# Kernel tuning notes

Measured on AMD Instinct MI355X. Metric: run time of the kernel, lower is better.

## Reference

```python
import jax, jax.numpy as jnp
import numpy as np

FEATURE_DIM = 1024
MAX_DEPTH = 32
HID = 128
N = 32768


def setup_inputs() -> dict:
    key = jax.random.key(0)
    ks = jax.random.split(key, 16)
    d = FEATURE_DIM
    s = 0.02
    return {
        "features": jax.random.normal(ks[0], (N, d), jnp.float32),
        "depths": jax.random.randint(ks[1], (N,), 0, MAX_DEPTH),
        "pos_emb": jax.random.normal(ks[2], (MAX_DEPTH, d), jnp.float32) * s,
        "aW1": jax.random.normal(ks[3], (HID, 2 * d), jnp.float32) * s,
        "ab1": jnp.zeros((HID,), jnp.float32),
        "aW2": jax.random.normal(ks[4], (1, HID), jnp.float32) * s,
        "ab2": jnp.zeros((1,), jnp.float32),
        "uW1": jax.random.normal(ks[5], (d, 2 * d), jnp.float32) * s,
        "ub1": jnp.zeros((d,), jnp.float32),
        "uW2": jax.random.normal(ks[6], (d, d), jnp.float32) * s,
        "ub2": jnp.zeros((d,), jnp.float32),
        "gW": jax.random.normal(ks[7], (d, 2 * d), jnp.float32) * s,
        "gb": jnp.zeros((d,), jnp.float32),
    }


def reference(features, depths, pos_emb, aW1, ab1, aW2, ab2,
              uW1, ub1, uW2, ub2, gW, gb):
    # add position embeddings (depths clamped to [0, MAX_DEPTH-1])
    dep = jnp.clip(depths, 0, MAX_DEPTH - 1)
    f = features + pos_emb[dep]                       # [N, d]
    target = f[0:1]                                    # [1, d]
    path = f[1:]                                       # [N-1, d]

    # attention MLP over all path states at once (vectorizes the torch loop)
    tb = jnp.broadcast_to(target, path.shape)          # [N-1, d]
    comb = jnp.concatenate([tb, path], axis=1)         # [N-1, 2d]
    h = jax.nn.relu(comb @ aW1.T + ab1)                # [N-1, 128]
    attn = jax.nn.sigmoid(h @ aW2.T + ab2)             # [N-1, 1]

    s = attn.sum()
    attn = jnp.where(s > 0, attn / s, attn)

    agg = (path * attn).sum(axis=0, keepdims=True)     # [1, d]
    c2 = jnp.concatenate([target, agg], axis=1)        # [1, 2d]
    gate = jax.nn.sigmoid(c2 @ gW.T + gb)
    upd = jax.nn.relu(c2 @ uW1.T + ub1) @ uW2.T + ub2
    updated_target = target + gate * upd
    return jnp.concatenate([updated_target, path], axis=0)
```

## Files before the change

kernel.cpp:

```cpp
#include <hip/hip_runtime.h>

#define DNUM 1024
#define HIDN 128
#define NTOT 32768
#define MR 32
#define NBLK 1024

#define T_OFF 0
#define P0_OFF 1024
#define S_OFF 1152
#define AGG_OFF 1216
#define GATE_OFF 2240
#define U1_OFF 3264
#define W2_FOFF 4288
#define AGGP_OFF (W2_FOFF + 65536)
#define SP_OFF (AGGP_OFF + NBLK * DNUM)
#define WS_NEED ((size_t)(SP_OFF + NBLK) * 4)

typedef __attribute__((ext_vector_type(8))) short short8;
typedef __attribute__((ext_vector_type(4))) float f32x4;

__device__ __forceinline__ unsigned short f2bf(float x) {
  unsigned int u = __builtin_bit_cast(unsigned int, x);
  u = u + 0x7fffu + ((u >> 16) & 1u);
  return (unsigned short)(u >> 16);
}
__device__ __forceinline__ float bf2f(unsigned int bits16) {
  unsigned int u = bits16 << 16;
  return __builtin_bit_cast(float, u);
}

__global__ __launch_bounds__(256) void ka(const float* __restrict__ features,
                                          const int* __restrict__ depths,
                                          const float* __restrict__ pos_emb,
                                          float* __restrict__ ws) {
  int t = threadIdx.x;
  int dep = depths[0];
  dep = dep < 0 ? 0 : (dep > 31 ? 31 : dep);
  float4 fv = *(const float4*)(features + t * 4);
  float4 pe = *(const float4*)(pos_emb + dep * DNUM + t * 4);
  float4 r;
  r.x = fv.x + pe.x; r.y = fv.y + pe.y; r.z = fv.z + pe.z; r.w = fv.w + pe.w;
  *(float4*)(ws + T_OFF + t * 4) = r;
  float4 z = make_float4(0.f, 0.f, 0.f, 0.f);
  *(float4*)(ws + AGG_OFF + t * 4) = z;
  if (t < 64) ws[S_OFF + t] = 0.f;
}

__global__ __launch_bounds__(256) void kaw(const float* __restrict__ aW1,
                                           const float* __restrict__ ab1,
                                           float* __restrict__ ws,
                                           unsigned short* __restrict__ w2) {
  int t = threadIdx.x, bid = blockIdx.x;
  if (bid == 0) {
    __shared__ float ph[256];
    int j = t >> 1, h = t & 1;
    const float* wrow = aW1 + (size_t)j * (2 * DNUM) + h * 512;
    const float* tr = ws + T_OFF + h * 512;
    float p = 0.f;
    for (int k = 0; k < 512; k += 4) {
      float4 wv = *(const float4*)(wrow + k);
      float4 tv = *(const float4*)(tr + k);
      p += wv.x * tv.x + wv.y * tv.y + wv.z * tv.z + wv.w * tv.w;
    }
    ph[t] = p;
    __syncthreads();
    if (t < HIDN) ws[P0_OFF + t] = ab1[t] + ph[t * 2] + ph[t * 2 + 1];
    return;
  }
  int idx = ((bid - 1) * 256 + t) * 4;
  int j = idx >> 10, k = idx & 1023;
  float4 v = *(const float4*)(aW1 + (size_t)j * 2048 + 1024 + k);
  uint2 pk;
  pk.x = (unsigned int)f2bf(v.x) | ((unsigned int)f2bf(v.y) << 16);
  pk.y = (unsigned int)f2bf(v.z) | ((unsigned int)f2bf(v.w) << 16);
  *(uint2*)(w2 + idx) = pk;
}

__global__ __launch_bounds__(512, 4) void kbig(
    const float* __restrict__ features, const int* __restrict__ depths,
    const float* __restrict__ pos_emb, const float* __restrict__ p0,
    const float* __restrict__ aW2, const float* __restrict__ ab2,
    const unsigned short* __restrict__ w2, float* __restrict__ out,
    float* __restrict__ agg, float* __restrict__ sacc,
    float* __restrict__ aggp, float* __restrict__ sp) {
  __shared__ __align__(16) unsigned char ldsA[MR * 2048];
  __shared__ int depsL[MR];
  __shared__ float part[160];
  __shared__ float comb[1024];
  const int t = threadIdx.x;
  const int bid = blockIdx.x;
  const int lane = t & 63;
  const int w = t >> 6;
  const int llo = lane & 15;
  const int lhi = lane >> 4;
  const int tc = t & 255;
  const int th = t >> 8;
  const int col = tc * 4;

  if (t < MR) {
    int fr = 1 + bid * MR + t;
    int dp = (fr < NTOT) ? depths[fr] : 0;
    dp = dp < 0 ? 0 : (dp > 31 ? 31 : dp);
    depsL[t] = dp;
  }
  __syncthreads();

#pragma unroll
  for (int g = 0; g < 2; ++g) {
    float4 fb[8];
#pragma unroll
    for (int q = 0; q < 8; ++q) {
      int i = (g * 8 + q) * 2 + th;
      int fr = 1 + bid * MR + i;
      fb[q] = (fr < NTOT) ? *(const float4*)(features + (size_t)fr * DNUM + col)
                          : make_float4(0.f, 0.f, 0.f, 0.f);
    }
#pragma unroll
    for (int q = 0; q < 8; ++q) {
      int i = (g * 8 + q) * 2 + th;
      int fr = 1 + bid * MR + i;
      float4 f = make_float4(0.f, 0.f, 0.f, 0.f);
      if (fr < NTOT) {
        float4 pe = *(const float4*)(pos_emb + depsL[i] * DNUM + col);
        f.x = fb[q].x + pe.x; f.y = fb[q].y + pe.y;
        f.z = fb[q].z + pe.z; f.w = fb[q].w + pe.w;
        *(float4*)(out + (size_t)fr * DNUM + col) = f;
      }
      uint2 pk;
      pk.x = (unsigned int)f2bf(f.x) | ((unsigned int)f2bf(f.y) << 16);
      pk.y = (unsigned int)f2bf(f.z) | ((unsigned int)f2bf(f.w) << 16);
      int off = (i * 2048 + tc * 8) ^ ((i & 7) << 4);
      *(uint2*)(ldsA + off) = pk;
    }
  }
  __syncthreads();

  const int wm = w >> 2, wn = w & 3;
  f32x4 acc[2];
  acc[0] = (f32x4){0.f, 0.f, 0.f, 0.f};
  acc[1] = (f32x4){0.f, 0.f, 0.f, 0.f};
  const int arow = wm * 16 + llo;
  const int abase = arow * 2048;
  const int aswz = (arow & 7) << 4;
  const unsigned short* bpA = w2 + (size_t)(wn * 32 + llo) * DNUM + lhi * 8;
  const unsigned short* bpB = bpA + 16 * DNUM;

#pragma unroll 4
  for (int kc = 0; kc < 32; ++kc) {
    int kbase = kc * 32;
    short8 av = *(short8*)(ldsA + ((abase + (kbase + lhi * 8) * 2) ^ aswz));
    short8 bv0 = *(const short8*)(bpA + kbase);
    short8 bv1 = *(const short8*)(bpB + kbase);
    acc[0] = __builtin_amdgcn_mfma_f32_16x16x32_bf16(av, bv0, acc[0], 0, 0, 0);
    acc[1] = __builtin_amdgcn_mfma_f32_16x16x32_bf16(av, bv1, acc[1], 0, 0, 0);
  }

  float p0v[2], wv[2];
#pragma unroll
  for (int n = 0; n < 2; ++n) {
    int j = wn * 32 + n * 16 + llo;
    p0v[n] = p0[j];
    wv[n] = aW2[j];
  }
#pragma unroll
  for (int e = 0; e < 4; ++e) {
    float s = 0.f;
#pragma unroll
    for (int n = 0; n < 2; ++n) {
      float h = acc[n][e] + p0v[n];
      h = fmaxf(h, 0.f);
      s += h * wv[n];
    }
    s += __shfl_xor(s, 1);
    s += __shfl_xor(s, 2);
    s += __shfl_xor(s, 4);
    s += __shfl_xor(s, 8);
    if (llo == 0) part[wn * 32 + wm * 16 + lhi * 4 + e] = s;
  }
  __syncthreads();

  if (t < MR) {
    float pre = part[t] + part[32 + t] + part[64 + t] + part[96 + t] + ab2[0];
    int fr = 1 + bid * MR + t;
    float raw = 0.f;
    if (fr < NTOT) raw = 1.f / (1.f + __expf(-pre));
    part[128 + t] = raw;
  }
  __syncthreads();

  float a0 = 0.f, a1 = 0.f, a2 = 0.f, a3 = 0.f;
  for (int lr = th * 16; lr < th * 16 + 16; ++lr) {
    float r = part[128 + lr];
    int off = (lr * 2048 + tc * 8) ^ ((lr & 7) << 4);
    uint2 pk = *(uint2*)(ldsA + off);
    a0 += r * bf2f(pk.x & 0xffffu);
    a1 += r * bf2f(pk.x >> 16);
    a2 += r * bf2f(pk.y & 0xffffu);
    a3 += r * bf2f(pk.y >> 16);
  }
  if (th == 1) {
    comb[tc * 4 + 0] = a0; comb[tc * 4 + 1] = a1;
    comb[tc * 4 + 2] = a2; comb[tc * 4 + 3] = a3;
  }
  __syncthreads();
  if (th == 0) {
    float c0 = a0 + comb[tc * 4 + 0];
    float c1 = a1 + comb[tc * 4 + 1];
    float c2v = a2 + comb[tc * 4 + 2];
    float c3 = a3 + comb[tc * 4 + 3];
    if (aggp) {
      f32x4 v = {c0, c1, c2v, c3};
      *(f32x4*)(aggp + (size_t)bid * DNUM + col) = v;
    } else {
      atomicAdd(agg + col + 0, c0);
      atomicAdd(agg + col + 1, c1);
      atomicAdd(agg + col + 2, c2v);
      atomicAdd(agg + col + 3, c3);
    }
  }
  if (t == 0) {
    float s = 0.f;
    for (int lr = 0; lr < MR; ++lr) s += part[128 + lr];
    if (sp) sp[bid] = s;
    else atomicAdd(sacc + (bid & 63), s);
  }
}

__global__ __launch_bounds__(256) void kred(const float* __restrict__ aggp,
                                            const float* __restrict__ sp,
                                            float* __restrict__ ws) {
  int t = threadIdx.x, bid = blockIdx.x;
  if (bid < 256) {
    int w = t >> 6, lane = t & 63;
    int colIdx = bid * 4 + w;
    float s = 0.f;
#pragma unroll 4
    for (int k = 0; k < 16; ++k) {
      int r = lane + k * 64;
      s += aggp[(size_t)r * DNUM + colIdx];
    }
    s += __shfl_xor(s, 1);
    s += __shfl_xor(s, 2);
    s += __shfl_xor(s, 4);
    s += __shfl_xor(s, 8);
    s += __shfl_xor(s, 16);
    s += __shfl_xor(s, 32);
    if (lane == 0) ws[AGG_OFF + colIdx] = s;
  } else {
    __shared__ float red[256];
    float s = sp[t] + sp[t + 256] + sp[t + 512] + sp[t + 768];
    red[t] = s;
    __syncthreads();
    if (t < 64) {
      float v = red[t] + red[t + 64] + red[t + 128] + red[t + 192];
      v += __shfl_xor(v, 1);
      v += __shfl_xor(v, 2);
      v += __shfl_xor(v, 4);
      v += __shfl_xor(v, 8);
      v += __shfl_xor(v, 16);
      v += __shfl_xor(v, 32);
      if (t == 0) ws[S_OFF] = v;
    }
  }
}

__global__ __launch_bounds__(256) void kc1(const float* __restrict__ gW,
                                           const float* __restrict__ gb,
                                           const float* __restrict__ uW1,
                                           const float* __restrict__ ub1,
                                           float* __restrict__ ws) {
  __shared__ float c2[2048];
  __shared__ float sinv_sh;
  int t = threadIdx.x, bid = blockIdx.x;
  if (t == 0) {
    float s = 0.f;
    for (int i = 0; i < 64; ++i) s += ws[S_OFF + i];
    sinv_sh = (s > 0.f) ? 1.f / s : 1.f;
  }
  __syncthreads();
  float sinv = sinv_sh;
  for (int i = t; i < 2048; i += 256)
    c2[i] = (i < 1024) ? ws[T_OFF + i] : ws[AGG_OFF + i - 1024] * sinv;
  __syncthreads();
  int w = t >> 6, lane = t & 63;
  int isGate = bid < 256;
  int o = (isGate ? bid : bid - 256) * 4 + w;
  const float* W = isGate ? gW : uW1;
  float p = 0.f;
  for (int i = lane; i < 2048; i += 64) p += W[(size_t)o * 2048 + i] * c2[i];
  p += __shfl_xor(p, 1);
  p += __shfl_xor(p, 2);
  p += __shfl_xor(p, 4);
  p += __shfl_xor(p, 8);
  p += __shfl_xor(p, 16);
  p += __shfl_xor(p, 32);
  if (lane == 0) {
    float v = p + (isGate ? gb[o] : ub1[o]);
    v = isGate ? (1.f / (1.f + expf(-v))) : fmaxf(v, 0.f);
    ws[(isGate ? GATE_OFF : U1_OFF) + o] = v;
  }
}

__global__ __launch_bounds__(256) void kc2(const float* __restrict__ uW2,
                                           const float* __restrict__ ub2,
                                           const float* __restrict__ ws,
                                           float* __restrict__ out) {
  __shared__ float u1[1024];
  int t = threadIdx.x, bid = blockIdx.x;
  for (int i = t; i < 1024; i += 256) u1[i] = ws[U1_OFF + i];
  __syncthreads();
  int w = t >> 6, lane = t & 63;
  int o = bid * 4 + w;
  float p = 0.f;
  for (int i = lane; i < 1024; i += 64) p += uW2[(size_t)o * 1024 + i] * u1[i];
  p += __shfl_xor(p, 1);
  p += __shfl_xor(p, 2);
  p += __shfl_xor(p, 4);
  p += __shfl_xor(p, 8);
  p += __shfl_xor(p, 16);
  p += __shfl_xor(p, 32);
  if (lane == 0) {
    float upd = p + ub2[o];
    out[o] = ws[T_OFF + o] + ws[GATE_OFF + o] * upd;
  }
}

extern "C" void kernel_launch(void* const* d_in, const int* in_sizes, int n_in,
                              void* d_out, int out_size, void* d_ws, size_t ws_size,
                              hipStream_t stream) {
  const float* features = (const float*)d_in[0];
  const int* depths = (const int*)d_in[1];
  const float* pos_emb = (const float*)d_in[2];
  const float* aW1 = (const float*)d_in[3];
  const float* ab1 = (const float*)d_in[4];
  const float* aW2 = (const float*)d_in[5];
  const float* ab2 = (const float*)d_in[6];
  const float* uW1 = (const float*)d_in[7];
  const float* ub1 = (const float*)d_in[8];
  const float* uW2 = (const float*)d_in[9];
  const float* ub2 = (const float*)d_in[10];
  const float* gW = (const float*)d_in[11];
  const float* gb = (const float*)d_in[12];
  float* out = (float*)d_out;
  float* ws = (float*)d_ws;
  unsigned short* w2 = (unsigned short*)(ws + W2_FOFF);
  bool useP = ws_size >= WS_NEED;
  float* aggp = useP ? (ws + AGGP_OFF) : nullptr;
  float* sp = useP ? (ws + SP_OFF) : nullptr;

  hipLaunchKernelGGL(ka, dim3(1), dim3(256), 0, stream, features, depths, pos_emb, ws);
  hipLaunchKernelGGL(kaw, dim3(129), dim3(256), 0, stream, aW1, ab1, ws, w2);
  hipLaunchKernelGGL(kbig, dim3(NBLK), dim3(512), 0, stream, features, depths, pos_emb,
                     ws + P0_OFF, aW2, ab2, w2, out, ws + AGG_OFF, ws + S_OFF, aggp, sp);
  if (useP)
    hipLaunchKernelGGL(kred, dim3(257), dim3(256), 0, stream, aggp, sp, ws);
  hipLaunchKernelGGL(kc1, dim3(512), dim3(256), 0, stream, gW, gb, uW1, ub1, ws);
  hipLaunchKernelGGL(kc2, dim3(256), dim3(256), 0, stream, uW2, ub2, ws, out);
}
```

Baseline: 179.1 us.

## Pipeline feature loads with MFMA via double-buffered LDS tiles per block

The main kernel now processes 64 rows per block in four 16-row tiles with double-buffered LDS. The global load of the next tile's features is issued before the current tile's MFMA/attention work, and its LDS write happens after, so memory latency overlaps compute. Each wave now covers 16 hidden units for 16 rows. The grid is halved to 512 blocks, which also halves the partial-aggregate buffer that the reduction kernel reads. In exchange there are more barriers per block, fewer blocks to fill the GPU, and fewer MFMA per wave per tile.

Result: no change. 182.5 us (+1.9%).

```diff
diff --git a/kernel.cpp b/kernel.cpp
--- a/kernel.cpp
+++ b/kernel.cpp
@@ -3,8 +3,10 @@
 #define DNUM 1024
 #define HIDN 128
 #define NTOT 32768
-#define MR 32
-#define NBLK 1024
+#define MR 16
+#define TB 4
+#define ROWS_PB (MR * TB)
+#define NBLKB 512
 
 #define T_OFF 0
 #define P0_OFF 1024
@@ -14,8 +16,8 @@
 #define U1_OFF 3264
 #define W2_FOFF 4288
 #define AGGP_OFF (W2_FOFF + 65536)
-#define SP_OFF (AGGP_OFF + NBLK * DNUM)
-#define WS_NEED ((size_t)(SP_OFF + NBLK) * 4)
+#define SP_OFF (AGGP_OFF + NBLKB * DNUM)
+#define WS_NEED ((size_t)(SP_OFF + NBLKB) * 4)
 
 typedef __attribute__((ext_vector_type(8))) short short8;
 typedef __attribute__((ext_vector_type(4))) float f32x4;
@@ -77,16 +79,15 @@
   *(uint2*)(w2 + idx) = pk;
 }
 
-__global__ __launch_bounds__(512, 4) void kbig(
+__global__ __launch_bounds__(512, 4) void kpipe(
     const float* __restrict__ features, const int* __restrict__ depths,
     const float* __restrict__ pos_emb, const float* __restrict__ p0,
     const float* __restrict__ aW2, const float* __restrict__ ab2,
     const unsigned short* __restrict__ w2, float* __restrict__ out,
     float* __restrict__ agg, float* __restrict__ sacc,
     float* __restrict__ aggp, float* __restrict__ sp) {
-  __shared__ __align__(16) unsigned char ldsA[MR * 2048];
-  __shared__ int depsL[MR];
-  __shared__ float part[160];
+  __shared__ __align__(16) unsigned char lds[2][MR * 2048];
+  __shared__ float part[144];
   __shared__ float comb[1024];
   const int t = threadIdx.x;
   const int bid = blockIdx.x;
@@ -97,32 +98,28 @@
   const int tc = t & 255;
   const int th = t >> 8;
   const int col = tc * 4;
-
-  if (t < MR) {
-    int fr = 1 + bid * MR + t;
-    int dp = (fr < NTOT) ? depths[fr] : 0;
-    dp = dp < 0 ? 0 : (dp > 31 ? 31 : dp);
-    depsL[t] = dp;
-  }
-  __syncthreads();
-
-#pragma unroll
-  for (int g = 0; g < 2; ++g) {
-    float4 fb[8];
+  const int rowbase = 1 + bid * ROWS_PB;
+
+  float4 fb[8];
+
+  auto FLOAD = [&](int tt) {
 #pragma unroll
     for (int q = 0; q < 8; ++q) {
-      int i = (g * 8 + q) * 2 + th;
-      int fr = 1 + bid * MR + i;
+      int fr = rowbase + tt * MR + q * 2 + th;
       fb[q] = (fr < NTOT) ? *(const float4*)(features + (size_t)fr * DNUM + col)
                           : make_float4(0.f, 0.f, 0.f, 0.f);
     }
+  };
+  auto WRITE = [&](int tt, unsigned char* buf) {
 #pragma unroll
     for (int q = 0; q < 8; ++q) {
-      int i = (g * 8 + q) * 2 + th;
-      int fr = 1 + bid * MR + i;
+      int i = q * 2 + th;
+      int fr = rowbase + tt * MR + i;
       float4 f = make_float4(0.f, 0.f, 0.f, 0.f);
       if (fr < NTOT) {
-        float4 pe = *(const float4*)(pos_emb + depsL[i] * DNUM + col);
+        int dp = depths[fr];
+        dp = dp < 0 ? 0 : (dp > 31 ? 31 : dp);
+        float4 pe = *(const float4*)(pos_emb + (size_t)dp * DNUM + col);
         f.x = fb[q].x + pe.x; f.y = fb[q].y + pe.y;
         f.z = fb[q].z + pe.z; f.w = fb[q].w + pe.w;
         *(float4*)(out + (size_t)fr * DNUM + col) = f;
@@ -131,74 +128,81 @@
       pk.x = (unsigned int)f2bf(f.x) | ((unsigned int)f2bf(f.y) << 16);
       pk.y = (unsigned int)f2bf(f.z) | ((unsigned int)f2bf(f.w) << 16);
       int off = (i * 2048 + tc * 8) ^ ((i & 7) << 4);
-      *(uint2*)(ldsA + off) = pk;
-    }
-  }
-  __syncthreads();
-
-  const int wm = w >> 2, wn = w & 3;
-  f32x4 acc[2];
-  acc[0] = (f32x4){0.f, 0.f, 0.f, 0.f};
-  acc[1] = (f32x4){0.f, 0.f, 0.f, 0.f};
-  const int arow = wm * 16 + llo;
-  const int abase = arow * 2048;
-  const int aswz = (arow & 7) << 4;
-  const unsigned short* bpA = w2 + (size_t)(wn * 32 + llo) * DNUM + lhi * 8;
-  const unsigned short* bpB = bpA + 16 * DNUM;
-
+      *(uint2*)(buf + off) = pk;
+    }
+  };
+
+  FLOAD(0);
+  WRITE(0, lds[0]);
+  __syncthreads();
+
+  const int jg = w * 16;
+  const float p0v = p0[jg + llo];
+  const float wv = aW2[jg + llo];
+  const float bias2 = ab2[0];
+  const unsigned short* bp = w2 + (size_t)(jg + llo) * DNUM + lhi * 8;
+  const int abase = llo * 2048;
+  const int aswz = (llo & 7) << 4;
+
+  float a0 = 0.f, a1 = 0.f, a2 = 0.f, a3 = 0.f;
+  float ssum = 0.f;
+
+  for (int tt = 0; tt < TB; ++tt) {
+    unsigned char* buf = lds[tt & 1];
+    if (tt + 1 < TB) FLOAD(tt + 1);
+
+    f32x4 acc = (f32x4){0.f, 0.f, 0.f, 0.f};
 #pragma unroll 4
-  for (int kc = 0; kc < 32; ++kc) {
-    int kbase = kc * 32;
-    short8 av = *(short8*)(ldsA + ((abase + (kbase + lhi * 8) * 2) ^ aswz));
-    short8 bv0 = *(const short8*)(bpA + kbase);
-    short8 bv1 = *(const short8*)(bpB + kbase);
-    acc[0] = __builtin_amdgcn_mfma_f32_16x16x32_bf16(av, bv0, acc[0], 0, 0, 0);
-    acc[1] = __builtin_amdgcn_mfma_f32_16x16x32_bf16(av, bv1, acc[1], 0, 0, 0);
-  }
-
-  float p0v[2], wv[2];
-#pragma unroll
-  for (int n = 0; n < 2; ++n) {
-    int j = wn * 32 + n * 16 + llo;
-    p0v[n] = p0[j];
-    wv[n] = aW2[j];
-  }
-#pragma unroll
-  for (int e = 0; e < 4; ++e) {
-    float s = 0.f;
-#pragma unroll
-    for (int n = 0; n < 2; ++n) {
-      float h = acc[n][e] + p0v[n];
-      h = fmaxf(h, 0.f);
-      s += h * wv[n];
-    }
-    s += __shfl_xor(s, 1);
-    s += __shfl_xor(s, 2);
-    s += __shfl_xor(s, 4);
-    s += __shfl_xor(s, 8);
-    if (llo == 0) part[wn * 32 + wm * 16 + lhi * 4 + e] = s;
-  }
-  __syncthreads();
-
-  if (t < MR) {
-    float pre = part[t] + part[32 + t] + part[64 + t] + part[96 + t] + ab2[0];
-    int fr = 1 + bid * MR + t;
-    float raw = 0.f;
-    if (fr < NTOT) raw = 1.f / (1.f + __expf(-pre));
-    part[128 + t] = raw;
-  }
-  __syncthreads();
-
-  float a0 = 0.f, a1 = 0.f, a2 = 0.f, a3 = 0.f;
-  for (int lr = th * 16; lr < th * 16 + 16; ++lr) {
-    float r = part[128 + lr];
-    int off = (lr * 2048 + tc * 8) ^ ((lr & 7) << 4);
-    uint2 pk = *(uint2*)(ldsA + off);
-    a0 += r * bf2f(pk.x & 0xffffu);
-    a1 += r * bf2f(pk.x >> 16);
-    a2 += r * bf2f(pk.y & 0xffffu);
-    a3 += r * bf2f(pk.y >> 16);
-  }
+    for (int kc = 0; kc < 32; ++kc) {
+      short8 av = *(short8*)(buf + ((abase + (kc * 32 + lhi * 8) * 2) ^ aswz));
+      short8 bv = *(const short8*)(bp + kc * 32);
+      acc = __builtin_amdgcn_mfma_f32_16x16x32_bf16(av, bv, acc, 0, 0, 0);
+    }
+
+#pragma unroll
+    for (int e = 0; e < 4; ++e) {
+      float h = fmaxf(acc[e] + p0v, 0.f);
+      float s = h * wv;
+      s += __shfl_xor(s, 1);
+      s += __shfl_xor(s, 2);
+      s += __shfl_xor(s, 4);
+      s += __shfl_xor(s, 8);
+      if (llo == 0) part[w * 16 + lhi * 4 + e] = s;
+    }
+    __syncthreads();
+
+    if (t < MR) {
+      float pre = bias2;
+#pragma unroll
+      for (int w8 = 0; w8 < 8; ++w8) pre += part[w8 * 16 + t];
+      int fr = rowbase + tt * MR + t;
+      float raw = 0.f;
+      if (fr < NTOT) raw = 1.f / (1.f + __expf(-pre));
+      part[128 + t] = raw;
+    }
+    __syncthreads();
+
+#pragma unroll
+    for (int lr2 = 0; lr2 < 8; ++lr2) {
+      int lr = th * 8 + lr2;
+      float r = part[128 + lr];
+      int off = (lr * 2048 + tc * 8) ^ ((lr & 7) << 4);
+      uint2 pk = *(uint2*)(buf + off);
+      a0 += r * bf2f(pk.x & 0xffffu);
+      a1 += r * bf2f(pk.x >> 16);
+      a2 += r * bf2f(pk.y & 0xffffu);
+      a3 += r * bf2f(pk.y >> 16);
+    }
+    if (t == 0) {
+      float s = 0.f;
+#pragma unroll
+      for (int i = 0; i < MR; ++i) s += part[128 + i];
+      ssum += s;
+    }
+    if (tt + 1 < TB) WRITE(tt + 1, lds[(tt + 1) & 1]);
+    __syncthreads();
+  }
+
   if (th == 1) {
     comb[tc * 4 + 0] = a0; comb[tc * 4 + 1] = a1;
     comb[tc * 4 + 2] = a2; comb[tc * 4 + 3] = a3;
@@ -220,10 +224,8 @@
     }
   }
   if (t == 0) {
-    float s = 0.f;
-    for (int lr = 0; lr < MR; ++lr) s += part[128 + lr];
-    if (sp) sp[bid] = s;
-    else atomicAdd(sacc + (bid & 63), s);
+    if (sp) sp[bid] = ssum;
+    else atomicAdd(sacc + (bid & 63), ssum);
   }
 }
 
@@ -236,7 +238,7 @@
     int colIdx = bid * 4 + w;
     float s = 0.f;
 #pragma unroll 4
-    for (int k = 0; k < 16; ++k) {
+    for (int k = 0; k < NBLKB / 64; ++k) {
       int r = lane + k * 64;
       s += aggp[(size_t)r * DNUM + colIdx];
     }
@@ -249,7 +251,8 @@
     if (lane == 0) ws[AGG_OFF + colIdx] = s;
   } else {
     __shared__ float red[256];
-    float s = sp[t] + sp[t + 256] + sp[t + 512] + sp[t + 768];
+    float s = 0.f;
+    for (int k = t; k < NBLKB; k += 256) s += sp[k];
     red[t] = s;
     __syncthreads();
     if (t < 64) {
@@ -351,8 +354,9 @@
 
   hipLaunchKernelGGL(ka, dim3(1), dim3(256), 0, stream, features, depths, pos_emb, ws);
   hipLaunchKernelGGL(kaw, dim3(129), dim3(256), 0, stream, aW1, ab1, ws, w2);
-  hipLaunchKernelGGL(kbig, dim3(NBLK), dim3(512), 0, stream, features, depths, pos_emb,
-                     ws + P0_OFF, aW2, ab2, w2, out, ws + AGG_OFF, ws + S_OFF, aggp, sp);
+  hipLaunchKernelGGL(kpipe, dim3(NBLKB), dim3(512), 0, stream,
+                     features, depths, pos_emb, ws + P0_OFF, aW2, ab2, w2, out,
+                     ws + AGG_OFF, ws + S_OFF, aggp, sp);
   if (useP)
     hipLaunchKernelGGL(kred, dim3(257), dim3(256), 0, stream, aggp, sp, ws);
   hipLaunchKernelGGL(kc1, dim3(512), dim3(256), 0, stream, gW, gb, uW1, ub1, ws);
```
